# Kernel tuning notes

Hardware: AMD Instinct MI355X
Metric: run time of the kernel (lower is better)

## Reference

```python
import jax, jax.numpy as jnp
import numpy as np

D_MODEL = 1024
HEADS = 16


def setup_inputs() -> dict:
    key = jax.random.key(0)
    ks = jax.random.split(key, 6)
    B, N, d = 4, 1024, D_MODEL
    s = 1.0 / np.sqrt(d)
    return {
        "x": jax.random.normal(ks[0], (B, N, d), dtype=jnp.float32),
        "attn_bias": jax.random.normal(ks[1], (B, HEADS, N, N), dtype=jnp.float32),
        "Wq": jax.random.normal(ks[2], (d, d), dtype=jnp.float32) * s,
        "Wk": jax.random.normal(ks[3], (d, d), dtype=jnp.float32) * s,
        "Wv": jax.random.normal(ks[4], (d, d), dtype=jnp.float32) * s,
        "Wo": jax.random.normal(ks[5], (d, d), dtype=jnp.float32) * s,
    }


def reference(x, attn_bias, Wq, Wk, Wv, Wo):
    B, N, d = x.shape
    H = HEADS
    hd = d // H
    # projections -> [B, H, N, hd] (torch Linear: x @ W.T)
    q = (x @ Wq.T).reshape(B, N, H, hd).transpose(0, 2, 1, 3)
    k = (x @ Wk.T).reshape(B, N, H, hd).transpose(0, 2, 1, 3)
    v = (x @ Wv.T).reshape(B, N, H, hd).transpose(0, 2, 1, 3)
    scale = hd ** -0.5
    attn = jnp.einsum('bhqd,bhkd->bhqk', q, k) * scale + attn_bias
    attn = jax.nn.softmax(attn, axis=-1)
    out = jnp.einsum('bhqk,bhkd->bhqd', attn, v)
    out = out.transpose(0, 2, 1, 3).reshape(B, N, d)
    return out @ Wo.T
```

## Files before the change

kernel.cpp:

```cpp
#include <hip/hip_runtime.h>
#include <hip/hip_bf16.h>
#include <math.h>


typedef __bf16 bf16;
typedef bf16 bf16x8 __attribute__((ext_vector_type(8)));
typedef bf16 bf16x4 __attribute__((ext_vector_type(4)));
typedef float floatx4 __attribute__((ext_vector_type(4)));

#define MFMA16(a, b, c) __builtin_amdgcn_mfma_f32_16x16x32_bf16((a), (b), (c), 0, 0, 0)

__device__ __forceinline__ void gload_lds16(const bf16* g, bf16* l) {
  __builtin_amdgcn_global_load_lds(
      (const __attribute__((address_space(1))) unsigned int*)g,
      (__attribute__((address_space(3))) unsigned int*)l, 16, 0, 0);
}

__global__ __launch_bounds__(256) void cvt_kernel(
    const float* __restrict__ x, const float* __restrict__ wq,
    const float* __restrict__ wk, const float* __restrict__ wv,
    const float* __restrict__ wo, bf16* __restrict__ dst) {
  long e = ((long)blockIdx.x * 256 + threadIdx.x) * 4;
  const float* src;
  if (e < 4194304) {
    src = x + e;
  } else {
    long r = (e - 4194304) >> 20;
    long off = (e - 4194304) & 1048575;
    src = (r == 0 ? wq : r == 1 ? wk : r == 2 ? wv : wo) + off;
  }
  float4 v = *reinterpret_cast<const float4*>(src);
  bf16x4 o = { (bf16)v.x, (bf16)v.y, (bf16)v.z, (bf16)v.w };
  *reinterpret_cast<bf16x4*>(dst + e) = o;
}

__device__ __forceinline__ void gemm_mainloop(const bf16* __restrict__ Ag,
                                              const bf16* __restrict__ Bg,
                                              bf16* As, bf16* Bs,
                                              floatx4 acc[4][4]) {
  int tid = threadIdx.x;
  int w = tid >> 6, l = tid & 63, g = l >> 4, ln = l & 15;
  int wr = (w >> 1) << 6, wc = (w & 1) << 6;
  int lrow = w * 16 + (l >> 2);
  int lkc = (l & 3) * 8;
  for (int k0 = 0; k0 < 1024; k0 += 32) {
    __syncthreads();
    gload_lds16(Ag + (size_t)lrow * 1024 + k0 + lkc, As + w * 512);
    gload_lds16(Ag + (size_t)(lrow + 64) * 1024 + k0 + lkc, As + 2048 + w * 512);
    gload_lds16(Bg + (size_t)lrow * 1024 + k0 + lkc, Bs + w * 512);
    gload_lds16(Bg + (size_t)(lrow + 64) * 1024 + k0 + lkc, Bs + 2048 + w * 512);
    asm volatile("s_waitcnt vmcnt(0)" ::: "memory");
    __syncthreads();
    bf16x8 af[4], bfv[4];
#pragma unroll
    for (int t = 0; t < 4; t++) {
      af[t] = *(const bf16x8*)&As[(wr + t * 16 + ln) * 32 + g * 8];
      bfv[t] = *(const bf16x8*)&Bs[(wc + t * 16 + ln) * 32 + g * 8];
    }
#pragma unroll
    for (int i = 0; i < 4; i++)
#pragma unroll
      for (int j = 0; j < 4; j++)
        acc[i][j] = MFMA16(af[i], bfv[j], acc[i][j]);
  }
}

__global__ __launch_bounds__(256) void qkv_proj(
    const bf16* __restrict__ xb, const bf16* __restrict__ wqkv,
    bf16* __restrict__ Qo, bf16* __restrict__ Ko, bf16* __restrict__ Vo) {
  __shared__ bf16 As[4096], Bs[4096];
  const floatx4 z4 = {0.f, 0.f, 0.f, 0.f};
  floatx4 acc[4][4];
#pragma unroll
  for (int i = 0; i < 4; i++)
#pragma unroll
    for (int j = 0; j < 4; j++) acc[i][j] = z4;
  int z = blockIdx.z;
  const bf16* Ag = xb + (size_t)blockIdx.x * 128 * 1024;
  const bf16* Bg = wqkv + (size_t)z * 1048576 + (size_t)blockIdx.y * 128 * 1024;
  gemm_mainloop(Ag, Bg, As, Bs, acc);
  bf16* dst = z == 0 ? Qo : (z == 1 ? Ko : Vo);
  int tid = threadIdx.x, w = tid >> 6, l = tid & 63, g = l >> 4, ln = l & 15;
  int mbase = blockIdx.x * 128 + ((w >> 1) << 6);
  int ibase = blockIdx.y * 128 + ((w & 1) << 6);
#pragma unroll
  for (int i = 0; i < 4; i++)
#pragma unroll
    for (int j = 0; j < 4; j++)
#pragma unroll
      for (int r = 0; r < 4; r++) {
        int m = mbase + i * 16 + g * 4 + r;
        int col = ibase + j * 16 + ln;
        int b = m >> 10, n = m & 1023, h = col >> 6, di = col & 63;
        dst[((size_t)((b * 16 + h) * 1024 + n) << 6) + di] = (bf16)acc[i][j][r];
      }
}

__global__ __launch_bounds__(256) void flash_kernel(
    const bf16* __restrict__ Q, const bf16* __restrict__ Kg,
    const bf16* __restrict__ Vg, const float* __restrict__ bias,
    bf16* __restrict__ Ao) {
  __shared__ bf16 Klds[64 * 72];
  __shared__ bf16 Vtlds[64 * 72];
  __shared__ bf16 Plds[4 * 16 * 72];
  int tid = threadIdx.x;
  int w = tid >> 6, l = tid & 63, g = l >> 4, ln = l & 15;
  int qt = blockIdx.x;
  int bh = blockIdx.y;
  size_t bhN = (size_t)bh * 1024;

  const bf16* qptr = Q + (bhN + qt * 64 + w * 16 + ln) * 64;
  bf16x8 qf0 = *(const bf16x8*)(qptr + g * 8);
  bf16x8 qf1 = *(const bf16x8*)(qptr + 32 + g * 8);

  const floatx4 z4 = {0.f, 0.f, 0.f, 0.f};
  floatx4 o[4];
  float m_i[4], l_i[4];
#pragma unroll
  for (int i = 0; i < 4; i++) { o[i] = z4; m_i[i] = -1e30f; l_i[i] = 0.f; }

  const float* bbase = bias + ((bhN + qt * 64 + w * 16 + g * 4) << 10) + ln;
  float bc[4][4];
#pragma unroll
  for (int t = 0; t < 4; t++)
#pragma unroll
    for (int r = 0; r < 4; r++) bc[t][r] = bbase[(size_t)r * 1024 + t * 16];

  bf16* pw = Plds + w * 16 * 72;
  int skey = l;
  int skc2 = w * 2;

  for (int kb = 0; kb < 16; kb++) {
    __syncthreads();
    const bf16* krow = Kg + (bhN + kb * 64 + skey) * 64;
    const bf16* vrow = Vg + (bhN + kb * 64 + skey) * 64;
#pragma unroll
    for (int c0 = 0; c0 < 2; c0++) {
      int kc = skc2 + c0;
      *(bf16x8*)&Klds[skey * 72 + kc * 8] = *(const bf16x8*)(krow + kc * 8);
      bf16x8 vv = *(const bf16x8*)(vrow + kc * 8);
#pragma unroll
      for (int j = 0; j < 8; j++) Vtlds[(kc * 8 + j) * 72 + skey] = vv[j];
    }
    __syncthreads();

    float bn[4][4];
    if (kb < 15) {
      const float* bp = bbase + (kb + 1) * 64;
#pragma unroll
      for (int t = 0; t < 4; t++)
#pragma unroll
        for (int r = 0; r < 4; r++) bn[t][r] = bp[(size_t)r * 1024 + t * 16];
    }

    floatx4 s[4];
#pragma unroll
    for (int t = 0; t < 4; t++) {
      s[t] = z4;
      bf16x8 kf0 = *(const bf16x8*)&Klds[(t * 16 + ln) * 72 + g * 8];
      bf16x8 kf1 = *(const bf16x8*)&Klds[(t * 16 + ln) * 72 + 32 + g * 8];
      s[t] = MFMA16(qf0, kf0, s[t]);
      s[t] = MFMA16(qf1, kf1, s[t]);
    }
#pragma unroll
    for (int t = 0; t < 4; t++)
#pragma unroll
      for (int r = 0; r < 4; r++)
        s[t][r] = fmaf(s[t][r], 0.125f, bc[t][r]);

    float cmax[4], rs[4], alpha[4];
#pragma unroll
    for (int r = 0; r < 4; r++)
      cmax[r] = fmaxf(fmaxf(s[0][r], s[1][r]), fmaxf(s[2][r], s[3][r]));
#pragma unroll
    for (int mk = 1; mk < 16; mk <<= 1)
#pragma unroll
      for (int r = 0; r < 4; r++)
        cmax[r] = fmaxf(cmax[r], __shfl_xor(cmax[r], mk, 64));
#pragma unroll
    for (int r = 0; r < 4; r++) {
      float mn = fmaxf(m_i[r], cmax[r]);
      alpha[r] = __expf(m_i[r] - mn);
      m_i[r] = mn;
      rs[r] = 0.f;
    }
#pragma unroll
    for (int t = 0; t < 4; t++)
#pragma unroll
      for (int r = 0; r < 4; r++) {
        float p = __expf(s[t][r] - m_i[r]);
        s[t][r] = p;
        rs[r] += p;
      }
#pragma unroll
    for (int mk = 1; mk < 16; mk <<= 1)
#pragma unroll
      for (int r = 0; r < 4; r++) rs[r] += __shfl_xor(rs[r], mk, 64);
#pragma unroll
    for (int r = 0; r < 4; r++) l_i[r] = l_i[r] * alpha[r] + rs[r];
#pragma unroll
    for (int dt = 0; dt < 4; dt++)
#pragma unroll
      for (int r = 0; r < 4; r++) o[dt][r] *= alpha[r];

#pragma unroll
    for (int t = 0; t < 4; t++)
#pragma unroll
      for (int r = 0; r < 4; r++)
        pw[(g * 4 + r) * 72 + t * 16 + ln] = (bf16)s[t][r];
    asm volatile("s_waitcnt lgkmcnt(0)" ::: "memory");

    bf16x8 pf0 = *(const bf16x8*)&pw[ln * 72 + g * 8];
    bf16x8 pf1 = *(const bf16x8*)&pw[ln * 72 + 32 + g * 8];
#pragma unroll
    for (int dt = 0; dt < 4; dt++) {
      bf16x8 vf0 = *(const bf16x8*)&Vtlds[(dt * 16 + ln) * 72 + g * 8];
      bf16x8 vf1 = *(const bf16x8*)&Vtlds[(dt * 16 + ln) * 72 + 32 + g * 8];
      o[dt] = MFMA16(pf0, vf0, o[dt]);
      o[dt] = MFMA16(pf1, vf1, o[dt]);
    }
#pragma unroll
    for (int t = 0; t < 4; t++)
#pragma unroll
      for (int r = 0; r < 4; r++) bc[t][r] = bn[t][r];
  }

  int b = bh >> 4, h = bh & 15;
#pragma unroll
  for (int r = 0; r < 4; r++) {
    float inv = 1.f / l_i[r];
    int row = b * 1024 + qt * 64 + w * 16 + g * 4 + r;
    bf16* op = Ao + (size_t)row * 1024 + h * 64 + ln;
#pragma unroll
    for (int dt = 0; dt < 4; dt++) op[dt * 16] = (bf16)(o[dt][r] * inv);
  }
}

__global__ __launch_bounds__(256) void out_proj(const bf16* __restrict__ Ab,
                                                const bf16* __restrict__ wob,
                                                float* __restrict__ C) {
  __shared__ bf16 As[4096], Bs[2048];
  const floatx4 z4 = {0.f, 0.f, 0.f, 0.f};
  floatx4 acc[4][2];
#pragma unroll
  for (int i = 0; i < 4; i++)
#pragma unroll
    for (int j = 0; j < 2; j++) acc[i][j] = z4;
  const bf16* Ag = Ab + (size_t)blockIdx.x * 128 * 1024;
  const bf16* Bg = wob + (size_t)blockIdx.y * 64 * 1024;
  int tid = threadIdx.x;
  int w = tid >> 6, l = tid & 63, g = l >> 4, ln = l & 15;
  int wr = (w >> 1) << 6, wc = (w & 1) << 5;
  int lrow = w * 16 + (l >> 2);
  int lkc = (l & 3) * 8;
  for (int k0 = 0; k0 < 1024; k0 += 32) {
    __syncthreads();
    gload_lds16(Ag + (size_t)lrow * 1024 + k0 + lkc, As + w * 512);
    gload_lds16(Ag + (size_t)(lrow + 64) * 1024 + k0 + lkc, As + 2048 + w * 512);
    gload_lds16(Bg + (size_t)lrow * 1024 + k0 + lkc, Bs + w * 512);
    asm volatile("s_waitcnt vmcnt(0)" ::: "memory");
    __syncthreads();
    bf16x8 af[4], bfv[2];
#pragma unroll
    for (int t = 0; t < 4; t++)
      af[t] = *(const bf16x8*)&As[(wr + t * 16 + ln) * 32 + g * 8];
#pragma unroll
    for (int t = 0; t < 2; t++)
      bfv[t] = *(const bf16x8*)&Bs[(wc + t * 16 + ln) * 32 + g * 8];
#pragma unroll
    for (int i = 0; i < 4; i++)
#pragma unroll
      for (int j = 0; j < 2; j++)
        acc[i][j] = MFMA16(af[i], bfv[j], acc[i][j]);
  }
  int mbase = blockIdx.x * 128 + wr;
  int cbase = blockIdx.y * 64 + wc;
#pragma unroll
  for (int i = 0; i < 4; i++)
#pragma unroll
    for (int j = 0; j < 2; j++)
#pragma unroll
      for (int r = 0; r < 4; r++)
        C[(size_t)(mbase + i * 16 + g * 4 + r) * 1024 + cbase + j * 16 + ln] =
            acc[i][j][r];
}

extern "C" void kernel_launch(void* const* d_in, const int* in_sizes, int n_in,
                              void* d_out, int out_size, void* d_ws, size_t ws_size,
                              hipStream_t stream) {
  const float* x = (const float*)d_in[0];
  const float* bias = (const float*)d_in[1];
  const float* Wq = (const float*)d_in[2];
  const float* Wk = (const float*)d_in[3];
  const float* Wv = (const float*)d_in[4];
  const float* Wo = (const float*)d_in[5];
  float* out = (float*)d_out;

  bf16* xb = (bf16*)d_ws;
  bf16* wqkv = xb + 4194304;
  bf16* wob = wqkv + 3 * 1048576;
  bf16* Qb = wob + 1048576;
  bf16* Kb = Qb + 4194304;
  bf16* Vb = Kb + 4194304;
  bf16* Ao = Vb + 4194304;

  cvt_kernel<<<8192, 256, 0, stream>>>(x, Wq, Wk, Wv, Wo, xb);
  qkv_proj<<<dim3(32, 8, 3), 256, 0, stream>>>(xb, wqkv, Qb, Kb, Vb);
  flash_kernel<<<dim3(16, 64), 256, 0, stream>>>(Qb, Kb, Vb, bias, Ao);
  out_proj<<<dim3(32, 16), 256, 0, stream>>>(Ao, wob, out);
}
```

Baseline: 504.0 us.

## Double-buffer K/V tiles in LDS with register prefetch in flash kernel

The flash attention kernel now prefetches the next K/V tile into registers at the start of each iteration and writes it into a second LDS buffer after the PV MFMAs. This cuts the two barriers per iteration down to one and hides global load latency behind compute. In exchange it doubles K/V LDS usage, which may lower occupancy, and adds register pressure from the prefetched tiles.

```diff
diff --git a/kernel.cpp b/kernel.cpp
--- a/kernel.cpp
+++ b/kernel.cpp
@@ -100,8 +100,8 @@
     const bf16* __restrict__ Q, const bf16* __restrict__ Kg,
     const bf16* __restrict__ Vg, const float* __restrict__ bias,
     bf16* __restrict__ Ao) {
-  __shared__ bf16 Klds[64 * 72];
-  __shared__ bf16 Vtlds[64 * 72];
+  __shared__ bf16 Klds[2][64 * 72];
+  __shared__ bf16 Vtlds[2][64 * 72];
   __shared__ bf16 Plds[4 * 16 * 72];
   int tid = threadIdx.x;
   int w = tid >> 6, l = tid & 63, g = l >> 4, ln = l & 15;
@@ -109,43 +109,55 @@
   int bh = blockIdx.y;
   size_t bhN = (size_t)bh * 1024;
 
+  int skey = l, skc2 = w * 2;
+  const bf16* Kbase = Kg + (bhN + skey) * 64;
+  const bf16* Vbase = Vg + (bhN + skey) * 64;
+
+  bf16x8 kr[2], vr[2];
+#pragma unroll
+  for (int c = 0; c < 2; c++) {
+    kr[c] = *(const bf16x8*)(Kbase + (skc2 + c) * 8);
+    vr[c] = *(const bf16x8*)(Vbase + (skc2 + c) * 8);
+  }
+
   const bf16* qptr = Q + (bhN + qt * 64 + w * 16 + ln) * 64;
   bf16x8 qf0 = *(const bf16x8*)(qptr + g * 8);
   bf16x8 qf1 = *(const bf16x8*)(qptr + 32 + g * 8);
 
+  const float* bbase = bias + ((bhN + qt * 64 + w * 16 + g * 4) << 10) + ln;
+  float bc[4][4];
+#pragma unroll
+  for (int t = 0; t < 4; t++)
+#pragma unroll
+    for (int r = 0; r < 4; r++) bc[t][r] = bbase[(size_t)r * 1024 + t * 16];
+
   const floatx4 z4 = {0.f, 0.f, 0.f, 0.f};
   floatx4 o[4];
   float m_i[4], l_i[4];
 #pragma unroll
   for (int i = 0; i < 4; i++) { o[i] = z4; m_i[i] = -1e30f; l_i[i] = 0.f; }
 
-  const float* bbase = bias + ((bhN + qt * 64 + w * 16 + g * 4) << 10) + ln;
-  float bc[4][4];
-#pragma unroll
-  for (int t = 0; t < 4; t++)
-#pragma unroll
-    for (int r = 0; r < 4; r++) bc[t][r] = bbase[(size_t)r * 1024 + t * 16];
+#pragma unroll
+  for (int c = 0; c < 2; c++) {
+    int kc = skc2 + c;
+    *(bf16x8*)&Klds[0][skey * 72 + kc * 8] = kr[c];
+#pragma unroll
+    for (int j = 0; j < 8; j++) Vtlds[0][(kc * 8 + j) * 72 + skey] = vr[c][j];
+  }
+  __syncthreads();
 
   bf16* pw = Plds + w * 16 * 72;
-  int skey = l;
-  int skc2 = w * 2;
-
+
+#pragma unroll 2
   for (int kb = 0; kb < 16; kb++) {
-    __syncthreads();
-    const bf16* krow = Kg + (bhN + kb * 64 + skey) * 64;
-    const bf16* vrow = Vg + (bhN + kb * 64 + skey) * 64;
-#pragma unroll
-    for (int c0 = 0; c0 < 2; c0++) {
-      int kc = skc2 + c0;
-      *(bf16x8*)&Klds[skey * 72 + kc * 8] = *(const bf16x8*)(krow + kc * 8);
-      bf16x8 vv = *(const bf16x8*)(vrow + kc * 8);
-#pragma unroll
-      for (int j = 0; j < 8; j++) Vtlds[(kc * 8 + j) * 72 + skey] = vv[j];
-    }
-    __syncthreads();
-
+    int cur = kb & 1, nxt = cur ^ 1;
     float bn[4][4];
     if (kb < 15) {
+#pragma unroll
+      for (int c = 0; c < 2; c++) {
+        kr[c] = *(const bf16x8*)(Kbase + (kb + 1) * 4096 + (skc2 + c) * 8);
+        vr[c] = *(const bf16x8*)(Vbase + (kb + 1) * 4096 + (skc2 + c) * 8);
+      }
       const float* bp = bbase + (kb + 1) * 64;
 #pragma unroll
       for (int t = 0; t < 4; t++)
@@ -157,8 +169,8 @@
 #pragma unroll
     for (int t = 0; t < 4; t++) {
       s[t] = z4;
-      bf16x8 kf0 = *(const bf16x8*)&Klds[(t * 16 + ln) * 72 + g * 8];
-      bf16x8 kf1 = *(const bf16x8*)&Klds[(t * 16 + ln) * 72 + 32 + g * 8];
+      bf16x8 kf0 = *(const bf16x8*)&Klds[cur][(t * 16 + ln) * 72 + g * 8];
+      bf16x8 kf1 = *(const bf16x8*)&Klds[cur][(t * 16 + ln) * 72 + 32 + g * 8];
       s[t] = MFMA16(qf0, kf0, s[t]);
       s[t] = MFMA16(qf1, kf1, s[t]);
     }
@@ -214,15 +226,27 @@
     bf16x8 pf1 = *(const bf16x8*)&pw[ln * 72 + 32 + g * 8];
 #pragma unroll
     for (int dt = 0; dt < 4; dt++) {
-      bf16x8 vf0 = *(const bf16x8*)&Vtlds[(dt * 16 + ln) * 72 + g * 8];
-      bf16x8 vf1 = *(const bf16x8*)&Vtlds[(dt * 16 + ln) * 72 + 32 + g * 8];
+      bf16x8 vf0 = *(const bf16x8*)&Vtlds[cur][(dt * 16 + ln) * 72 + g * 8];
+      bf16x8 vf1 = *(const bf16x8*)&Vtlds[cur][(dt * 16 + ln) * 72 + 32 + g * 8];
       o[dt] = MFMA16(pf0, vf0, o[dt]);
       o[dt] = MFMA16(pf1, vf1, o[dt]);
     }
-#pragma unroll
-    for (int t = 0; t < 4; t++)
-#pragma unroll
-      for (int r = 0; r < 4; r++) bc[t][r] = bn[t][r];
+
+    if (kb < 15) {
+#pragma unroll
+      for (int c = 0; c < 2; c++) {
+        int kc = skc2 + c;
+        *(bf16x8*)&Klds[nxt][skey * 72 + kc * 8] = kr[c];
+#pragma unroll
+        for (int j = 0; j < 8; j++)
+          Vtlds[nxt][(kc * 8 + j) * 72 + skey] = vr[c][j];
+      }
+#pragma unroll
+      for (int t = 0; t < 4; t++)
+#pragma unroll
+        for (int r = 0; r < 4; r++) bc[t][r] = bn[t][r];
+      __syncthreads();
+    }
   }
 
   int b = bh >> 4, h = bh & 15;
```

After: 461.0 us. -8.5%, faster.
